# Performance work log

Hardware: AMD Instinct MI355X
Metric: run time of the kernel (lower is better)

The kernel has to match this reference:

```python
import jax, jax.numpy as jnp
import numpy as np

N_NODES = 50000
N_EDGES = 800000
IN_FEAT = 128
N_HEADS = 4
OUT_FEAT = 16
NEG_SLOPE = 0.2


def setup_inputs() -> dict:
    key = jax.random.key(0)
    k1, k2, k3, k4, k5 = jax.random.split(key, 5)
    x = jax.random.normal(k1, (N_NODES, IN_FEAT), dtype=jnp.float32)
    src = jax.random.randint(k2, (N_EDGES,), 0, N_NODES)
    dst = jax.random.randint(k3, (N_EDGES,), 0, N_NODES)
    edge_index = jnp.stack([src, dst]).astype(jnp.int64)
    # xavier-uniform-like init for params
    limW = np.sqrt(6.0 / (IN_FEAT + N_HEADS * OUT_FEAT))
    W = jax.random.uniform(k4, (IN_FEAT, N_HEADS * OUT_FEAT), minval=-limW, maxval=limW, dtype=jnp.float32)
    lima = np.sqrt(6.0 / (N_HEADS + 2 * OUT_FEAT))
    a = jax.random.uniform(k5, (1, N_HEADS, 2 * OUT_FEAT), minval=-lima, maxval=lima, dtype=jnp.float32)
    return {"x": x, "edge_index": edge_index, "W": W, "a": a}


def reference(x, edge_index, W, a):
    N = x.shape[0]
    H = a.shape[1]
    F = a.shape[2] // 2
    src, dst = edge_index[0], edge_index[1]
    # node projection: [N, H, F]
    h = (x @ W).reshape(N, H, F)
    # split attention vector: sum(a * cat(h_src, h_dst)) = a_src.h_src + a_dst.h_dst
    a_src = a[0, :, :F]  # [H, F]
    a_dst = a[0, :, F:]  # [H, F]
    e_src = jnp.einsum('nhf,hf->nh', h, a_src)  # [N, H]
    e_dst = jnp.einsum('nhf,hf->nh', h, a_dst)  # [N, H]
    edge_e = jax.nn.leaky_relu(e_src[src] + e_dst[dst], NEG_SLOPE)  # [E, H]
    # softmax over heads (dim=1 in the source)
    alpha = jax.nn.softmax(edge_e, axis=1)  # [E, H]
    # dropout is identity in eval mode
    msg = alpha[:, :, None] * h[src]  # [E, H, F]
    out = jax.ops.segment_sum(msg, dst, num_segments=N)  # [N, H, F]
    # concat=True
    return out.reshape(N, H * F)
```

## Files before the change

kernel.cpp:

```cpp
#include <hip/hip_runtime.h>
#include <hip/hip_bf16.h>

#define IN_FEAT 128
#define N_HEADS 4
#define OUT_FEAT 16
#define HF 64
#define NEG_SLOPE 0.2f

#define BSHIFT 7
#define BNODES 128
#define NBUCK_MAX 512

typedef __hip_bfloat16 bf16;
typedef __attribute__((ext_vector_type(8))) short short8;
typedef __attribute__((ext_vector_type(4))) float f32x4;

__device__ inline unsigned short f2b(float f) {
  bf16 b = __float2bfloat16(f);
  return *(unsigned short*)&b;
}
__device__ inline float b2f(unsigned short u) {
  return __uint_as_float((unsigned)u << 16);
}
__device__ inline float alpha_lane(unsigned lo, unsigned hi, unsigned sel) {
  unsigned wd = (sel & 2u) ? hi : lo;
  return __uint_as_float(((wd >> ((sel & 1u) * 16u)) & 0xffffu) << 16);
}

__global__ __launch_bounds__(256) void k_gemm(
    const float* __restrict__ x, const float* __restrict__ W,
    const float* __restrict__ a, unsigned short* __restrict__ h16,
    float* __restrict__ e_src, float* __restrict__ e_dst,
    const int* __restrict__ dst, int* __restrict__ bh,
    int n_nodes, int n_edges, int nbuck, int chunkE, int gb) {
  __shared__ unsigned short xs[64][136];
  __shared__ unsigned short wt[64][136];
  __shared__ unsigned short sh[64][68];
  __shared__ int bhist[NBUCK_MAX];
  const int t = threadIdx.x;
  const int nb = blockIdx.x * 64;
  const int lane = t & 63;
  const int w = t >> 6;

  for (int i = t; i < NBUCK_MAX; i += 256) bhist[i] = 0;

  const float4* x4 = (const float4*)x;
  for (int i = t; i < 64 * 32; i += 256) {
    int n = i >> 5, k4 = i & 31;
    int gn = nb + n;
    float4 v = (gn < n_nodes) ? x4[(size_t)gn * 32 + k4]
                              : make_float4(0.f, 0.f, 0.f, 0.f);
    ushort4 u;
    u.x = f2b(v.x); u.y = f2b(v.y); u.z = f2b(v.z); u.w = f2b(v.w);
    *(ushort4*)&xs[n][k4 * 4] = u;
  }
  for (int i = t; i < IN_FEAT * HF; i += 256) {
    int k = i >> 6, c = i & 63;
    wt[c][k] = f2b(W[i]);
  }
  __syncthreads();

  const int m = lane & 15;
  const int q = lane >> 4;
  f32x4 acc[4];
#pragma unroll
  for (int nt = 0; nt < 4; ++nt) acc[nt] = (f32x4){0.f, 0.f, 0.f, 0.f};

#pragma unroll
  for (int kc = 0; kc < 4; ++kc) {
    short8 af = *(const short8*)&xs[w * 16 + m][kc * 32 + q * 8];
#pragma unroll
    for (int nt = 0; nt < 4; ++nt) {
      short8 bfr = *(const short8*)&wt[nt * 16 + m][kc * 32 + q * 8];
      acc[nt] = __builtin_amdgcn_mfma_f32_16x16x32_bf16(af, bfr, acc[nt], 0, 0, 0);
    }
  }

#pragma unroll
  for (int nt = 0; nt < 4; ++nt)
#pragma unroll
    for (int r = 0; r < 4; ++r)
      sh[w * 16 + q * 4 + r][nt * 16 + m] = f2b(acc[nt][r]);
  __syncthreads();

  {
    int n = t >> 2, hd = t & 3;
    int gn = nb + n;
    if (gn < n_nodes) {
      float es = 0.f, ed = 0.f;
#pragma unroll
      for (int f = 0; f < OUT_FEAT; ++f) {
        float hv = b2f(sh[n][hd * 16 + f]);
        es = fmaf(hv, a[hd * 2 * OUT_FEAT + f], es);
        ed = fmaf(hv, a[hd * 2 * OUT_FEAT + OUT_FEAT + f], ed);
      }
      e_src[gn * N_HEADS + hd] = es;
      e_dst[gn * N_HEADS + hd] = ed;
    }
  }

  for (int i = t; i < 64 * 16; i += 256) {
    int n = i >> 4, c4 = (i & 15) * 4;
    int gn = nb + n;
    if (gn < n_nodes) {
      ushort4 v;
      v.x = sh[n][c4 + 0]; v.y = sh[n][c4 + 1];
      v.z = sh[n][c4 + 2]; v.w = sh[n][c4 + 3];
      *(ushort4*)(h16 + (size_t)gn * HF + c4) = v;
    }
  }

  {
    int ebeg = blockIdx.x * chunkE;
    int eend = min(ebeg + chunkE, n_edges);
    for (int e = ebeg + t; e < eend; e += 256)
      atomicAdd(&bhist[dst[e] >> BSHIFT], 1);
    __syncthreads();
    for (int k = t; k < nbuck; k += 256)
      bh[(size_t)k * gb + blockIdx.x] = bhist[k];
  }
}

__global__ __launch_bounds__(1024) void k_scanA(
    const int* __restrict__ bh, int* __restrict__ sbase, int* __restrict__ tot,
    int gb) {
  __shared__ int s[1024];
  int t = threadIdx.x, k = blockIdx.x;
  int v = (t < gb) ? bh[(size_t)k * gb + t] : 0;
  s[t] = v;
  __syncthreads();
  for (int off = 1; off < 1024; off <<= 1) {
    int u = (t >= off) ? s[t - off] : 0;
    __syncthreads();
    s[t] += u;
    __syncthreads();
  }
  if (t < gb) sbase[(size_t)k * gb + t] = s[t] - v;
  if (t == 1023) tot[k] = s[t];
}

__global__ __launch_bounds__(512) void k_scanB(
    const int* __restrict__ tot, int* __restrict__ bucket_base,
    int* __restrict__ offsets, int nbuck, int n_edges, int n_nodes) {
  __shared__ int s[512];
  int t = threadIdx.x;
  int v = (t < nbuck) ? tot[t] : 0;
  s[t] = v;
  __syncthreads();
  for (int off = 1; off < 512; off <<= 1) {
    int u = (t >= off) ? s[t - off] : 0;
    __syncthreads();
    s[t] += u;
    __syncthreads();
  }
  if (t < nbuck) bucket_base[t] = s[t] - v;
  if (t == 0) {
    bucket_base[nbuck] = n_edges;
    offsets[n_nodes] = n_edges;
  }
}

__global__ __launch_bounds__(256) void k_part(
    const int* __restrict__ src, const int* __restrict__ dst,
    const float* __restrict__ e_src, const float* __restrict__ e_dst,
    const int* __restrict__ bucket_base, const int* __restrict__ sbase,
    uint4* __restrict__ recs, int nbuck, int chunkE, int n_edges, int gb) {
  __shared__ int cur[NBUCK_MAX];
  int t = threadIdx.x;
  for (int k = t; k < nbuck; k += 256)
    cur[k] = bucket_base[k] + sbase[(size_t)k * gb + blockIdx.x];
  __syncthreads();
  int beg = blockIdx.x * chunkE;
  int end = min(beg + chunkE, n_edges);
  for (int e = beg + t; e < end; e += 256) {
    int s = src[e], d = dst[e];
    float4 es = ((const float4*)e_src)[s];
    float4 ed = ((const float4*)e_dst)[d];
    float v0 = es.x + ed.x, v1 = es.y + ed.y, v2 = es.z + ed.z, v3 = es.w + ed.w;
    v0 = (v0 > 0.f) ? v0 : NEG_SLOPE * v0;
    v1 = (v1 > 0.f) ? v1 : NEG_SLOPE * v1;
    v2 = (v2 > 0.f) ? v2 : NEG_SLOPE * v2;
    v3 = (v3 > 0.f) ? v3 : NEG_SLOPE * v3;
    float m = fmaxf(fmaxf(v0, v1), fmaxf(v2, v3));
    float e0 = __expf(v0 - m), e1 = __expf(v1 - m);
    float e2 = __expf(v2 - m), e3 = __expf(v3 - m);
    float inv = 1.f / (e0 + e1 + e2 + e3);
    unsigned lo = (unsigned)f2b(e0 * inv) | ((unsigned)f2b(e1 * inv) << 16);
    unsigned hi = (unsigned)f2b(e2 * inv) | ((unsigned)f2b(e3 * inv) << 16);
    int pos = atomicAdd(&cur[d >> BSHIFT], 1);
    recs[pos] = make_uint4((unsigned)s, (unsigned)(d & (BNODES - 1)), lo, hi);
  }
}

__global__ __launch_bounds__(512) void k_sort(
    const uint4* __restrict__ recs, const int* __restrict__ bucket_base,
    uint4* __restrict__ sorted16, int* __restrict__ offsets,
    int nbuck, int n_nodes) {
  __shared__ int hist[BNODES];
  __shared__ int cur[BNODES];
  int t = threadIdx.x, k = blockIdx.x;
  int beg = bucket_base[k];
  int n = bucket_base[k + 1] - beg;
  if (t < BNODES) hist[t] = 0;
  __syncthreads();
  for (int j = t; j < n; j += 512)
    atomicAdd(&hist[recs[beg + j].y], 1);
  __syncthreads();
  int v = (t < BNODES) ? hist[t] : 0;
  for (int off = 1; off < BNODES; off <<= 1) {
    int u = (t < BNODES && t >= off) ? hist[t - off] : 0;
    __syncthreads();
    if (t < BNODES) hist[t] += u;
    __syncthreads();
  }
  if (t < BNODES) {
    int pos = beg + hist[t] - v;
    cur[t] = pos;
    int node = (k << BSHIFT) + t;
    if (node < n_nodes) offsets[node] = pos;
  }
  __syncthreads();
  for (int j = t; j < n; j += 512) {
    uint4 r = recs[beg + j];
    int p = atomicAdd(&cur[r.y], 1);
    sorted16[p] = make_uint4(r.x, 0u, r.z, r.w);
  }
}

__global__ __launch_bounds__(256) void k_gather(
    const uint4* __restrict__ sorted16, const int* __restrict__ offsets,
    const unsigned short* __restrict__ h16, float* __restrict__ out,
    int n_nodes) {
  int gid = blockIdx.x * 256 + threadIdx.x;
  int d = gid >> 6;
  int c = gid & 63;
  if (d >= n_nodes) return;
  int beg = offsets[d];
  int end = offsets[d + 1];
  unsigned sel = (unsigned)(c >> 4);
  float acc = 0.f;
  int j = beg;
  for (; j + 8 <= end; j += 8) {
    uint4 r[8];
    float hv[8];
#pragma unroll
    for (int k = 0; k < 8; ++k) r[k] = sorted16[j + k];
#pragma unroll
    for (int k = 0; k < 8; ++k) hv[k] = b2f(h16[(size_t)r[k].x * HF + c]);
#pragma unroll
    for (int k = 0; k < 8; ++k)
      acc = fmaf(alpha_lane(r[k].z, r[k].w, sel), hv[k], acc);
  }
  for (; j < end; ++j) {
    uint4 r = sorted16[j];
    acc = fmaf(alpha_lane(r.z, r.w, sel), b2f(h16[(size_t)r.x * HF + c]), acc);
  }
  out[(size_t)d * HF + c] = acc;
}

extern "C" void kernel_launch(void* const* d_in, const int* in_sizes, int n_in,
                              void* d_out, int out_size, void* d_ws, size_t ws_size,
                              hipStream_t stream) {
  const float* x = (const float*)d_in[0];
  const int* ei = (const int*)d_in[1];
  const float* W = (const float*)d_in[2];
  const float* a = (const float*)d_in[3];
  float* out = (float*)d_out;

  const int n_nodes = in_sizes[0] / IN_FEAT;
  const int n_edges = in_sizes[1] / 2;
  const int* src = ei;
  const int* dst = ei + n_edges;

  const int nbuck = (n_nodes + BNODES - 1) >> BSHIFT;
  const int gb = (n_nodes + 63) / 64;
  const int chunkE = (n_edges + gb - 1) / gb;

  char* ws = (char*)d_ws;
  size_t off = 0;
  uint4* recs = (uint4*)(ws + off);        off += (size_t)n_edges * 16;
  uint4* sorted16 = (uint4*)(ws + off);    off += (size_t)n_edges * 16;
  unsigned short* h16 = (unsigned short*)(ws + off); off += (size_t)n_nodes * HF * 2;
  float* e_src = (float*)(ws + off);       off += (size_t)n_nodes * N_HEADS * 4;
  float* e_dst = (float*)(ws + off);       off += (size_t)n_nodes * N_HEADS * 4;
  int* bh = (int*)(ws + off);              off += (size_t)NBUCK_MAX * gb * 4;
  int* sbase = (int*)(ws + off);           off += (size_t)NBUCK_MAX * gb * 4;
  int* tot = (int*)(ws + off);             off += (size_t)NBUCK_MAX * 4;
  int* bucket_base = (int*)(ws + off);     off += (size_t)(NBUCK_MAX + 1) * 4;
  int* offsets = (int*)(ws + off);         off += ((size_t)n_nodes + 16) * 4;

  k_gemm<<<gb, 256, 0, stream>>>(x, W, a, h16, e_src, e_dst, dst, bh,
                                 n_nodes, n_edges, nbuck, chunkE, gb);
  k_scanA<<<nbuck, 1024, 0, stream>>>(bh, sbase, tot, gb);
  k_scanB<<<1, 512, 0, stream>>>(tot, bucket_base, offsets, nbuck, n_edges, n_nodes);
  k_part<<<gb, 256, 0, stream>>>(src, dst, e_src, e_dst, bucket_base, sbase,
                                 recs, nbuck, chunkE, n_edges, gb);
  k_sort<<<nbuck, 512, 0, stream>>>(recs, bucket_base, sorted16, offsets, nbuck, n_nodes);
  k_gather<<<((size_t)n_nodes * 64 + 255) / 256, 256, 0, stream>>>(
      sorted16, offsets, h16, out, n_nodes);
}
```

Measured before the change: 170.3 us.

## Split gather wavefront into two half-waves over edges with paired bf16 loads

The gather kernel now has each lane load two bf16 features as one 32-bit word. The two 32-lane halves of a wavefront process alternating edges, and their partial sums are combined with a cross-lane shuffle. This halves the per-edge load instructions and doubles edges in flight, at the cost of clamped reads and masked work at tail boundaries. The sort kernel's histogram and scatter loops are also unrolled by four to increase memory-level parallelism.

```diff
diff --git a/kernel.cpp b/kernel.cpp
--- a/kernel.cpp
+++ b/kernel.cpp
@@ -21,10 +21,6 @@
 }
 __device__ inline float b2f(unsigned short u) {
   return __uint_as_float((unsigned)u << 16);
-}
-__device__ inline float alpha_lane(unsigned lo, unsigned hi, unsigned sel) {
-  unsigned wd = (sel & 2u) ? hi : lo;
-  return __uint_as_float(((wd >> ((sel & 1u) * 16u)) & 0xffffu) << 16);
 }
 
 __global__ __launch_bounds__(256) void k_gemm(
@@ -203,8 +199,20 @@
   int n = bucket_base[k + 1] - beg;
   if (t < BNODES) hist[t] = 0;
   __syncthreads();
-  for (int j = t; j < n; j += 512)
-    atomicAdd(&hist[recs[beg + j].y], 1);
+  {
+    int j = t;
+    for (; j + 1536 < n; j += 2048) {
+      unsigned y0 = recs[beg + j].y;
+      unsigned y1 = recs[beg + j + 512].y;
+      unsigned y2 = recs[beg + j + 1024].y;
+      unsigned y3 = recs[beg + j + 1536].y;
+      atomicAdd(&hist[y0], 1);
+      atomicAdd(&hist[y1], 1);
+      atomicAdd(&hist[y2], 1);
+      atomicAdd(&hist[y3], 1);
+    }
+    for (; j < n; j += 512) atomicAdd(&hist[recs[beg + j].y], 1);
+  }
   __syncthreads();
   int v = (t < BNODES) ? hist[t] : 0;
   for (int off = 1; off < BNODES; off <<= 1) {
@@ -220,10 +228,27 @@
     if (node < n_nodes) offsets[node] = pos;
   }
   __syncthreads();
-  for (int j = t; j < n; j += 512) {
-    uint4 r = recs[beg + j];
-    int p = atomicAdd(&cur[r.y], 1);
-    sorted16[p] = make_uint4(r.x, 0u, r.z, r.w);
+  {
+    int j = t;
+    for (; j + 1536 < n; j += 2048) {
+      uint4 r0 = recs[beg + j];
+      uint4 r1 = recs[beg + j + 512];
+      uint4 r2 = recs[beg + j + 1024];
+      uint4 r3 = recs[beg + j + 1536];
+      int p0 = atomicAdd(&cur[r0.y], 1);
+      int p1 = atomicAdd(&cur[r1.y], 1);
+      int p2 = atomicAdd(&cur[r2.y], 1);
+      int p3 = atomicAdd(&cur[r3.y], 1);
+      sorted16[p0] = make_uint4(r0.x, 0u, r0.z, r0.w);
+      sorted16[p1] = make_uint4(r1.x, 0u, r1.z, r1.w);
+      sorted16[p2] = make_uint4(r2.x, 0u, r2.z, r2.w);
+      sorted16[p3] = make_uint4(r3.x, 0u, r3.z, r3.w);
+    }
+    for (; j < n; j += 512) {
+      uint4 r = recs[beg + j];
+      int p = atomicAdd(&cur[r.y], 1);
+      sorted16[p] = make_uint4(r.x, 0u, r.z, r.w);
+    }
   }
 }
 
@@ -233,29 +258,44 @@
     int n_nodes) {
   int gid = blockIdx.x * 256 + threadIdx.x;
   int d = gid >> 6;
-  int c = gid & 63;
   if (d >= n_nodes) return;
+  int lane = threadIdx.x & 63;
+  int half = lane >> 5;
+  int c2 = lane & 31;
+  unsigned sel = (unsigned)(c2 >> 3);
+  unsigned shamt = (sel & 1u) * 16u;
   int beg = offsets[d];
   int end = offsets[d + 1];
-  unsigned sel = (unsigned)(c >> 4);
-  float acc = 0.f;
-  int j = beg;
-  for (; j + 8 <= end; j += 8) {
+  const unsigned* h32 = (const unsigned*)h16;
+  float a0 = 0.f, a1 = 0.f;
+  for (int j = beg; j < end; j += 16) {
     uint4 r[8];
-    float hv[8];
-#pragma unroll
-    for (int k = 0; k < 8; ++k) r[k] = sorted16[j + k];
-#pragma unroll
-    for (int k = 0; k < 8; ++k) hv[k] = b2f(h16[(size_t)r[k].x * HF + c]);
+#pragma unroll
+    for (int k = 0; k < 8; ++k) {
+      int idx = j + 2 * k + half;
+      int cidx = (idx < end) ? idx : (end - 1);
+      r[k] = sorted16[cidx];
+    }
+    unsigned hv[8];
 #pragma unroll
     for (int k = 0; k < 8; ++k)
-      acc = fmaf(alpha_lane(r[k].z, r[k].w, sel), hv[k], acc);
-  }
-  for (; j < end; ++j) {
-    uint4 r = sorted16[j];
-    acc = fmaf(alpha_lane(r.z, r.w, sel), b2f(h16[(size_t)r.x * HF + c]), acc);
-  }
-  out[(size_t)d * HF + c] = acc;
+      hv[k] = h32[(size_t)r[k].x * (HF / 2) + c2];
+#pragma unroll
+    for (int k = 0; k < 8; ++k) {
+      int idx = j + 2 * k + half;
+      unsigned wd = (sel & 2u) ? r[k].w : r[k].z;
+      float al = __uint_as_float(((wd >> shamt) & 0xffffu) << 16);
+      al = (idx < end) ? al : 0.f;
+      a0 = fmaf(al, b2f((unsigned short)(hv[k] & 0xffffu)), a0);
+      a1 = fmaf(al, b2f((unsigned short)(hv[k] >> 16)), a1);
+    }
+  }
+  a0 += __shfl_xor(a0, 32);
+  a1 += __shfl_xor(a1, 32);
+  if (half == 0) {
+    float2 v = make_float2(a0, a1);
+    *(float2*)(out + (size_t)d * HF + 2 * c2) = v;
+  }
 }
 
 extern "C" void kernel_launch(void* const* d_in, const int* in_sizes, int n_in,
```

Result: faster. 161.1 us (median of 2 runs) (-5.4%).

## Replace per-bucket sort and gather with shared-memory atomic aggregation per bucket

Applied to the files above, without the earlier changes.

Removes the counting-sort kernel and the per-node gather kernel. A single kernel now processes each 128-node destination bucket, accumulating alpha-weighted bf16 features into a padded LDS accumulator with float atomics, then writes the bucket's output rows. This drops one full pass that writes and re-reads the edge records, plus the offsets array, but adds many LDS atomic adds and makes float summation order nondeterministic. Parallelism is limited to one 1024-thread block per bucket (about 391 blocks).

```diff
diff --git a/kernel.cpp b/kernel.cpp
--- a/kernel.cpp
+++ b/kernel.cpp
@@ -10,6 +10,7 @@
 #define BSHIFT 7
 #define BNODES 128
 #define NBUCK_MAX 512
+#define APAD 65
 
 typedef __hip_bfloat16 bf16;
 typedef __attribute__((ext_vector_type(8))) short short8;
@@ -21,10 +22,6 @@
 }
 __device__ inline float b2f(unsigned short u) {
   return __uint_as_float((unsigned)u << 16);
-}
-__device__ inline float alpha_lane(unsigned lo, unsigned hi, unsigned sel) {
-  unsigned wd = (sel & 2u) ? hi : lo;
-  return __uint_as_float(((wd >> ((sel & 1u) * 16u)) & 0xffffu) << 16);
 }
 
 __global__ __launch_bounds__(256) void k_gemm(
@@ -136,12 +133,12 @@
     __syncthreads();
   }
   if (t < gb) sbase[(size_t)k * gb + t] = s[t] - v;
-  if (t == 1023) tot[k] = s[t];
+  if (t == 1023) tot[k] = s[1023];
 }
 
 __global__ __launch_bounds__(512) void k_scanB(
     const int* __restrict__ tot, int* __restrict__ bucket_base,
-    int* __restrict__ offsets, int nbuck, int n_edges, int n_nodes) {
+    int nbuck, int n_edges) {
   __shared__ int s[512];
   int t = threadIdx.x;
   int v = (t < nbuck) ? tot[t] : 0;
@@ -154,10 +151,7 @@
     __syncthreads();
   }
   if (t < nbuck) bucket_base[t] = s[t] - v;
-  if (t == 0) {
-    bucket_base[nbuck] = n_edges;
-    offsets[n_nodes] = n_edges;
-  }
+  if (t == 0) bucket_base[nbuck] = n_edges;
 }
 
 __global__ __launch_bounds__(256) void k_part(
@@ -192,70 +186,55 @@
   }
 }
 
-__global__ __launch_bounds__(512) void k_sort(
+__global__ __launch_bounds__(1024) void k_agg(
     const uint4* __restrict__ recs, const int* __restrict__ bucket_base,
-    uint4* __restrict__ sorted16, int* __restrict__ offsets,
-    int nbuck, int n_nodes) {
-  __shared__ int hist[BNODES];
-  __shared__ int cur[BNODES];
-  int t = threadIdx.x, k = blockIdx.x;
-  int beg = bucket_base[k];
-  int n = bucket_base[k + 1] - beg;
-  if (t < BNODES) hist[t] = 0;
-  __syncthreads();
-  for (int j = t; j < n; j += 512)
-    atomicAdd(&hist[recs[beg + j].y], 1);
-  __syncthreads();
-  int v = (t < BNODES) ? hist[t] : 0;
-  for (int off = 1; off < BNODES; off <<= 1) {
-    int u = (t < BNODES && t >= off) ? hist[t - off] : 0;
-    __syncthreads();
-    if (t < BNODES) hist[t] += u;
-    __syncthreads();
-  }
-  if (t < BNODES) {
-    int pos = beg + hist[t] - v;
-    cur[t] = pos;
-    int node = (k << BSHIFT) + t;
-    if (node < n_nodes) offsets[node] = pos;
-  }
-  __syncthreads();
-  for (int j = t; j < n; j += 512) {
-    uint4 r = recs[beg + j];
-    int p = atomicAdd(&cur[r.y], 1);
-    sorted16[p] = make_uint4(r.x, 0u, r.z, r.w);
-  }
-}
-
-__global__ __launch_bounds__(256) void k_gather(
-    const uint4* __restrict__ sorted16, const int* __restrict__ offsets,
     const unsigned short* __restrict__ h16, float* __restrict__ out,
     int n_nodes) {
-  int gid = blockIdx.x * 256 + threadIdx.x;
-  int d = gid >> 6;
-  int c = gid & 63;
-  if (d >= n_nodes) return;
-  int beg = offsets[d];
-  int end = offsets[d + 1];
-  unsigned sel = (unsigned)(c >> 4);
-  float acc = 0.f;
-  int j = beg;
-  for (; j + 8 <= end; j += 8) {
-    uint4 r[8];
-    float hv[8];
-#pragma unroll
-    for (int k = 0; k < 8; ++k) r[k] = sorted16[j + k];
-#pragma unroll
-    for (int k = 0; k < 8; ++k) hv[k] = b2f(h16[(size_t)r[k].x * HF + c]);
-#pragma unroll
-    for (int k = 0; k < 8; ++k)
-      acc = fmaf(alpha_lane(r[k].z, r[k].w, sel), hv[k], acc);
-  }
-  for (; j < end; ++j) {
-    uint4 r = sorted16[j];
-    acc = fmaf(alpha_lane(r.z, r.w, sel), b2f(h16[(size_t)r.x * HF + c]), acc);
-  }
-  out[(size_t)d * HF + c] = acc;
+  __shared__ float acc[BNODES * APAD];
+  const int t = threadIdx.x;
+  const int k = blockIdx.x;
+  for (int i = t; i < BNODES * APAD; i += 1024) acc[i] = 0.f;
+  __syncthreads();
+  const int beg = bucket_base[k];
+  const int end = bucket_base[k + 1];
+  const int w = t >> 6;
+  const int lane = t & 63;
+  const int p = lane >> 4;
+  const int q = lane & 15;
+  const unsigned sel = (unsigned)(q >> 2);
+  const unsigned shamt = (sel & 1u) * 16u;
+  const uint2* h2 = (const uint2*)h16;
+
+  for (int j0 = beg + w * 16; j0 < end; j0 += 256) {
+#pragma unroll
+    for (int u = 0; u < 4; ++u) {
+      int idx = j0 + u * 4 + p;
+      int cidx = (idx < end) ? idx : (end - 1);
+      uint4 r = recs[cidx];
+      uint2 hv = h2[(size_t)r.x * (HF / 4) + q];
+      unsigned wd = (sel & 2u) ? r.w : r.z;
+      float al = __uint_as_float(((wd >> shamt) & 0xffffu) << 16);
+      al = (idx < end) ? al : 0.f;
+      float* arow = &acc[(int)r.y * APAD + 4 * q];
+      atomicAdd(&arow[0], al * b2f((unsigned short)(hv.x & 0xffffu)));
+      atomicAdd(&arow[1], al * b2f((unsigned short)(hv.x >> 16)));
+      atomicAdd(&arow[2], al * b2f((unsigned short)(hv.y & 0xffffu)));
+      atomicAdd(&arow[3], al * b2f((unsigned short)(hv.y >> 16)));
+    }
+  }
+  __syncthreads();
+
+  const int base_node = k << BSHIFT;
+  float4* out4 = (float4*)out;
+  for (int i = t; i < BNODES * (HF / 4); i += 1024) {
+    int row = i >> 4, c4 = i & 15;
+    int node = base_node + row;
+    if (node < n_nodes) {
+      const float* ar = &acc[row * APAD + c4 * 4];
+      out4[(size_t)node * (HF / 4) + c4] =
+          make_float4(ar[0], ar[1], ar[2], ar[3]);
+    }
+  }
 }
 
 extern "C" void kernel_launch(void* const* d_in, const int* in_sizes, int n_in,
@@ -279,7 +258,6 @@
   char* ws = (char*)d_ws;
   size_t off = 0;
   uint4* recs = (uint4*)(ws + off);        off += (size_t)n_edges * 16;
-  uint4* sorted16 = (uint4*)(ws + off);    off += (size_t)n_edges * 16;
   unsigned short* h16 = (unsigned short*)(ws + off); off += (size_t)n_nodes * HF * 2;
   float* e_src = (float*)(ws + off);       off += (size_t)n_nodes * N_HEADS * 4;
   float* e_dst = (float*)(ws + off);       off += (size_t)n_nodes * N_HEADS * 4;
@@ -287,15 +265,12 @@
   int* sbase = (int*)(ws + off);           off += (size_t)NBUCK_MAX * gb * 4;
   int* tot = (int*)(ws + off);             off += (size_t)NBUCK_MAX * 4;
   int* bucket_base = (int*)(ws + off);     off += (size_t)(NBUCK_MAX + 1) * 4;
-  int* offsets = (int*)(ws + off);         off += ((size_t)n_nodes + 16) * 4;
 
   k_gemm<<<gb, 256, 0, stream>>>(x, W, a, h16, e_src, e_dst, dst, bh,
                                  n_nodes, n_edges, nbuck, chunkE, gb);
   k_scanA<<<nbuck, 1024, 0, stream>>>(bh, sbase, tot, gb);
-  k_scanB<<<1, 512, 0, stream>>>(tot, bucket_base, offsets, nbuck, n_edges, n_nodes);
+  k_scanB<<<1, 512, 0, stream>>>(tot, bucket_base, nbuck, n_edges);
   k_part<<<gb, 256, 0, stream>>>(src, dst, e_src, e_dst, bucket_base, sbase,
                                  recs, nbuck, chunkE, n_edges, gb);
-  k_sort<<<nbuck, 512, 0, stream>>>(recs, bucket_base, sorted16, offsets, nbuck, n_nodes);
-  k_gather<<<((size_t)n_nodes * 64 + 255) / 256, 256, 0, stream>>>(
-      sorted16, offsets, h16, out, n_nodes);
-}
+  k_agg<<<nbuck, 1024, 0, stream>>>(recs, bucket_base, h16, out, n_nodes);
+}
```

Measured after the change: 469.4 us. 2.76x slower.
